# Optimization experiments

Measured on AMD Instinct MI355X. Metric: run time of the kernel, lower is better.

The kernel has to match this reference:

```python
import jax, jax.numpy as jnp
import numpy as np

B, T, V, E, H, N = 8, 128, 32000, 128, 256, 20
SHARPEN = 5.0
EPS = 1e-8  # torch cosine_similarity eps


def setup_inputs() -> dict:
    key = jax.random.key(0)
    ks = jax.random.split(key, 8)
    g = lambda k, shape, scale: (jax.random.normal(k, shape, dtype=jnp.float32) * scale)
    return {
        "x_ids": jax.random.randint(ks[0], (B, T), 0, V),
        "emb": g(ks[1], (V, E), 0.02),                 # nn.Embedding weight
        "W_i": g(ks[2], (H, E), E ** -0.5),            # rnn_i weight (no bias)
        "W_h": g(ks[3], (H, H), H ** -0.5),            # rnn_h weight
        "W_fc": g(ks[4], (V, 2 * H), (2 * H) ** -0.5), # fc -> vocab (softmaxed)
        "W_ops": g(ks[5], (3, 2 * H), (2 * H) ** -0.5),
        "W_choose": g(ks[6], (2, 2 * H), (2 * H) ** -0.5),
        "sharp": jnp.array([SHARPEN], dtype=jnp.float32),
    }


def _l2norm(x, eps=1e-12):
    # F.normalize(x, dim=-1)
    n = jnp.linalg.norm(x, axis=-1, keepdims=True)
    return x / jnp.maximum(n, eps)


def reference(x_ids, emb, W_i, W_h, W_fc, W_ops, W_choose, sharp):
    x = emb[x_ids]                                   # [B,T,E]
    # pre-normalize vocab rows for cosine-sim readout (clamped like torch)
    emb_cn = emb / jnp.maximum(jnp.linalg.norm(emb, axis=1, keepdims=True), EPS)
    sh = sharp[0]

    stack0 = jnp.full((B, N, E), 0.001, dtype=x.dtype)      # zero_offset + 0.001
    ptr0 = jnp.zeros((B, N), x.dtype).at[:, 0].set(1.0)     # pointer at slot 0
    h0 = jnp.zeros((B, H), x.dtype)

    def step(carry, xi):
        h, stack, ptr = carry
        ri = _l2norm(xi) @ W_i.T                     # rnn_i(normalize(x_t))
        h = jnp.tanh(ri + h @ W_h.T)
        hm = 1.0 - jax.nn.relu(h)
        hmod = jnp.concatenate([hm, hm], axis=1)     # [B,2H]
        # GumbelSoftmax(temp=1, hard=False) -> deterministic softmax (no noise)
        ops = jax.nn.softmax(hmod @ W_ops.T, axis=1)  # [B,3]
        push, pop, nop = ops[:, 0], ops[:, 1], ops[:, 2]
        # --- differentiable stack push/pop/nop ---
        pop_val = jnp.einsum('bn,bne->be', ptr, stack)      # soft read at pointer
        p_push = jnp.roll(ptr, 1, axis=1)
        p_pop = jnp.roll(ptr, -1, axis=1)
        new_ptr = push[:, None] * p_push + pop[:, None] * p_pop + nop[:, None] * ptr
        new_ptr = jnp.clip(new_ptr, EPS) ** sh              # sharpen
        new_ptr = new_ptr / jnp.sum(new_ptr, axis=1, keepdims=True)
        w = (push[:, None] * p_push)[:, :, None]            # write weight [B,N,1]
        new_stack = stack * (1.0 - w) + w * xi[:, None, :]
        # --- readout ---
        semantic = jax.nn.softmax(hmod @ W_fc.T, axis=1)    # [B,V]
        pv_n = pop_val / jnp.maximum(
            jnp.linalg.norm(pop_val, axis=1, keepdims=True), EPS)
        syntactic = pv_n @ emb_cn.T                          # cosine sim [B,V]
        choice = jax.nn.softmax(hmod @ W_choose.T, axis=1)   # [B,2]
        out = choice[:, 0:1] * semantic + choice[:, 1:2] * syntactic
        return (h, new_stack, new_ptr), out

    _, outs = jax.lax.scan(step, (h0, stack0, ptr0), jnp.swapaxes(x, 0, 1))
    return jnp.swapaxes(outs, 0, 1)  # [B,T,V]
```

## Files before the change

kernel.cpp:

```cpp
#include <hip/hip_runtime.h>
#include <hip/hip_bf16.h>
#include <stdint.h>

#define T_ 128
#define B_ 8
#define V_ 32000
#define E_ 128
#define H_ 256
#define N_ 20
#define M_ 1024
#define PIT 264
#define PIT2 136
#define NCH5 500

typedef __attribute__((ext_vector_type(8))) short short8;
typedef __attribute__((ext_vector_type(4))) float f32x4;
typedef unsigned short ushort;

static __device__ __forceinline__ ushort f2bf_u(float f) {
  __hip_bfloat16 h = __float2bfloat16(f);
  return *reinterpret_cast<ushort*>(&h);
}

__global__ void whb_k(const float* __restrict__ Wh, uint4* __restrict__ whb4) {
  int idx = blockIdx.x*256 + threadIdx.x;
  int k8 = idx >> 8, i = idx & 255;
  const float* s = Wh + i*H_ + k8*8;
  uint4 o;
  o.x = (uint32_t)f2bf_u(s[0]) | ((uint32_t)f2bf_u(s[1]) << 16);
  o.y = (uint32_t)f2bf_u(s[2]) | ((uint32_t)f2bf_u(s[3]) << 16);
  o.z = (uint32_t)f2bf_u(s[4]) | ((uint32_t)f2bf_u(s[5]) << 16);
  o.w = (uint32_t)f2bf_u(s[6]) | ((uint32_t)f2bf_u(s[7]) << 16);
  whb4[idx] = o;
}

__global__ void wit_k(const float* __restrict__ Wi, float* __restrict__ WiT) {
  int idx = blockIdx.x*256 + threadIdx.x;
  if (idx < H_*E_) {
    int i = idx >> 7, e = idx & (E_-1);
    WiT[e*H_ + i] = Wi[idx];
  }
}

__global__ void embn_k(const float* __restrict__ emb, ushort* __restrict__ embnb) {
  int v = blockIdx.x, l = threadIdx.x;
  float e0 = emb[v*E_ + l];
  float e1 = emb[v*E_ + 64 + l];
  float ss = e0*e0 + e1*e1;
  #pragma unroll
  for (int off = 32; off >= 1; off >>= 1) ss += __shfl_xor(ss, off);
  float inv = 1.f / fmaxf(sqrtf(ss), 1e-8f);
  embnb[v*E_ + l]      = f2bf_u(e0*inv);
  embnb[v*E_ + 64 + l] = f2bf_u(e1*inv);
}

__global__ void foldfc_k(const float* __restrict__ Wfc, ushort* __restrict__ Wfcb) {
  int idx = blockIdx.x*256 + threadIdx.x;
  int n = idx >> 8, k = idx & 255;
  Wfcb[idx] = f2bf_u(Wfc[n*2*H_ + k] + Wfc[n*2*H_ + H_ + k]);
}

__global__ __launch_bounds__(256) void ri_k(const int* __restrict__ x_ids,
    const float* __restrict__ emb, const float* __restrict__ WiT,
    float* __restrict__ RI)
{
  __shared__ float xn[E_];
  __shared__ float red[2];
  int r = blockIdx.x, tid = threadIdx.x;
  int id = x_ids[r];
  float v = 0.f;
  if (tid < E_) v = emb[id*E_ + tid];
  float ss = v*v;
  if (tid < E_) {
    #pragma unroll
    for (int off = 32; off >= 1; off >>= 1) ss += __shfl_xor(ss, off);
    if ((tid & 63) == 0) red[tid >> 6] = ss;
  }
  __syncthreads();
  float inv = 1.f / fmaxf(sqrtf(red[0] + red[1]), 1e-12f);
  if (tid < E_) xn[tid] = v*inv;
  __syncthreads();
  float s = 0.f;
  for (int e = 0; e < E_; ++e) s += xn[e]*WiT[e*H_ + tid];
  RI[r*H_ + tid] = s;
}

__global__ __launch_bounds__(1024) void chain_k(
    const uint4* __restrict__ whb4, const float* __restrict__ RI,
    float* __restrict__ HMf, ushort* __restrict__ HMb)
{
  __shared__ uint4 wlds[32*256];
  __shared__ __align__(16) float hbuf[2][H_];
  __shared__ float hred[3][H_];
  const int b = blockIdx.x, tid = threadIdx.x;
  const int q = tid >> 8, i = tid & 255;

  for (int m = tid; m < 32*256; m += 1024) wlds[m] = whb4[m];
  if (q == 0) hbuf[0][i] = 0.f;
  __syncthreads();
  float ri_c = (q == 0) ? RI[(size_t)b*T_*H_ + i] : 0.f;

  for (int t = 0; t < T_; ++t) {
    const int r = b*T_ + t;
    float ri_n = 0.f;
    if (q == 0 && t+1 < T_) ri_n = RI[(size_t)(r+1)*H_ + i];
    const float4* h4 = reinterpret_cast<const float4*>(hbuf[t & 1]);
    float p0 = 0.f, p1 = 0.f, p2 = 0.f, p3 = 0.f;
    #pragma unroll
    for (int j = 0; j < 8; ++j) {
      uint4 w = wlds[(q*8 + j)*256 + i];
      float4 ha = h4[q*16 + 2*j];
      float4 hb = h4[q*16 + 2*j + 1];
      p0 += __uint_as_float(w.x << 16)*ha.x + __uint_as_float(w.x & 0xffff0000u)*ha.y;
      p1 += __uint_as_float(w.y << 16)*ha.z + __uint_as_float(w.y & 0xffff0000u)*ha.w;
      p2 += __uint_as_float(w.z << 16)*hb.x + __uint_as_float(w.z & 0xffff0000u)*hb.y;
      p3 += __uint_as_float(w.w << 16)*hb.z + __uint_as_float(w.w & 0xffff0000u)*hb.w;
    }
    float p = (p0 + p1) + (p2 + p3);
    if (q) hred[q-1][i] = p;
    __syncthreads();
    if (q == 0) {
      float s = ri_c + p + hred[0][i] + hred[1][i] + hred[2][i];
      float hn = tanhf(s);
      hbuf[(t+1) & 1][i] = hn;
      float hm = 1.f - fmaxf(hn, 0.f);
      HMf[(size_t)r*H_ + i] = hm;
      HMb[(size_t)r*H_ + i] = f2bf_u(hm);
    }
    ri_c = ri_n;
    __syncthreads();
  }
}

__global__ __launch_bounds__(256) void stats5_k(const ushort* __restrict__ HMb,
    const ushort* __restrict__ Wfcb, const float* __restrict__ HMf,
    const float* __restrict__ W_ops, const float* __restrict__ W_ch,
    const float* __restrict__ sharp, const int* __restrict__ x_ids,
    const float* __restrict__ emb,
    float* __restrict__ SS, float* __restrict__ CH, float* __restrict__ PV,
    ushort* __restrict__ PVNb)
{
  __shared__ __align__(16) char smem[64*PIT*2];
  const int tid = threadIdx.x;
  const int wave = tid >> 6, lane = tid & 63;
  const int lr = lane & 15, g = lane >> 4;

  if (blockIdx.y == 0) {
    if (blockIdx.x >= B_) return;
    float*  ops_l = (float*)smem;
    float2* pw_l  = (float2*)(smem + 2048);
    int*    ids_l = (int*)(smem + 2048 + 20480);
    const int b = blockIdx.x;
    float wo[5][4];
    #pragma unroll
    for (int k = 0; k < 3; ++k)
      #pragma unroll
      for (int j = 0; j < 4; ++j)
        wo[k][j] = W_ops[k*2*H_ + 4*lane + j] + W_ops[k*2*H_ + H_ + 4*lane + j];
    #pragma unroll
    for (int k = 0; k < 2; ++k)
      #pragma unroll
      for (int j = 0; j < 4; ++j)
        wo[3+k][j] = W_ch[k*2*H_ + 4*lane + j] + W_ch[k*2*H_ + H_ + 4*lane + j];
    if (tid < T_) ids_l[tid] = x_ids[b*T_ + tid];
    for (int rl = wave*32; rl < wave*32 + 32; ++rl) {
      int R = b*T_ + rl;
      float4 hm4 = reinterpret_cast<const float4*>(HMf + (size_t)R*H_)[lane];
      float d0 = hm4.x*wo[0][0] + hm4.y*wo[0][1] + hm4.z*wo[0][2] + hm4.w*wo[0][3];
      float d1 = hm4.x*wo[1][0] + hm4.y*wo[1][1] + hm4.z*wo[1][2] + hm4.w*wo[1][3];
      float d2 = hm4.x*wo[2][0] + hm4.y*wo[2][1] + hm4.z*wo[2][2] + hm4.w*wo[2][3];
      float d3 = hm4.x*wo[3][0] + hm4.y*wo[3][1] + hm4.z*wo[3][2] + hm4.w*wo[3][3];
      float d4 = hm4.x*wo[4][0] + hm4.y*wo[4][1] + hm4.z*wo[4][2] + hm4.w*wo[4][3];
      #pragma unroll
      for (int off = 32; off >= 1; off >>= 1) {
        d0 += __shfl_xor(d0, off); d1 += __shfl_xor(d1, off); d2 += __shfl_xor(d2, off);
        d3 += __shfl_xor(d3, off); d4 += __shfl_xor(d4, off);
      }
      if (lane == 0) {
        float mx = fmaxf(d0, fmaxf(d1, d2));
        float e0 = expf(d0-mx), e1 = expf(d1-mx), e2 = expf(d2-mx);
        float oi = 1.f/(e0+e1+e2);
        ops_l[rl*4+0] = e0*oi; ops_l[rl*4+1] = e1*oi; ops_l[rl*4+2] = e2*oi;
        float cm = fmaxf(d3, d4);
        float f0 = expf(d3-cm), f1 = expf(d4-cm);
        float ci = 1.f/(f0+f1);
        CH[R*2] = f0*ci; CH[R*2+1] = f1*ci;
      }
    }
    __syncthreads();
    if (tid < 64) {
      const float sh = sharp[0];
      float ptr = (tid == 0) ? 1.f : 0.f;
      const int lp = (tid + N_ - 1) % N_, ln = (tid + 1) % N_;
      for (int t = 0; t < T_; ++t) {
        float push = ops_l[t*4+0], pop = ops_l[t*4+1], nop = ops_l[t*4+2];
        float pp = __shfl(ptr, lp);
        float po = __shfl(ptr, ln);
        float wgt = push*pp;
        float raw = wgt + pop*po + nop*ptr;
        float np = 0.f;
        if (tid < N_) np = exp2f(sh * log2f(fmaxf(raw, 1e-8f)));
        float ssum = np;
        #pragma unroll
        for (int off = 1; off < 32; off <<= 1) ssum += __shfl_xor(ssum, off);
        if (tid < N_) {
          pw_l[t*N_ + tid] = make_float2(ptr, wgt);
          ptr = np / ssum;
        }
      }
    }
    __syncthreads();
    if (tid < E_) {
      const int e = tid;
      float stck[N_];
      #pragma unroll
      for (int n = 0; n < N_; ++n) stck[n] = 0.001f;
      float xi_c = emb[(size_t)ids_l[0]*E_ + e];
      for (int t = 0; t < T_; ++t) {
        float xi_n = (t+1 < T_) ? emb[(size_t)ids_l[t+1]*E_ + e] : 0.f;
        float pv = 0.f;
        #pragma unroll
        for (int n = 0; n < N_; ++n) {
          float2 pw = pw_l[t*N_ + n];
          pv += pw.x * stck[n];
          stck[n] += pw.y * (xi_c - stck[n]);
        }
        PV[(size_t)(b*T_ + t)*E_ + e] = pv;
        xi_c = xi_n;
      }
    }
    __threadfence_block();
    __syncthreads();
    for (int rl = wave*32; rl < wave*32 + 32; ++rl) {
      int R = b*T_ + rl;
      float a = PV[(size_t)R*E_ + lane];
      float c = PV[(size_t)R*E_ + 64 + lane];
      float ss = a*a + c*c;
      #pragma unroll
      for (int off = 32; off >= 1; off >>= 1) ss += __shfl_xor(ss, off);
      float inv = 1.f / fmaxf(sqrtf(ss), 1e-8f);
      PVNb[(size_t)R*E_ + lane]      = f2bf_u(a*inv);
      PVNb[(size_t)R*E_ + 64 + lane] = f2bf_u(c*inv);
    }
    return;
  }

  ushort* Bs = (ushort*)smem;
  const int Cb = blockIdx.x*64;
  {
    const uint4* srcB = (const uint4*)(Wfcb + (size_t)Cb*H_);
    #pragma unroll
    for (int it = 0; it < 8; ++it) {
      int idx = it*256 + tid, row = idx >> 5, c = idx & 31;
      *(uint4*)&Bs[row*PIT + c*8] = srcB[row*32 + c];
    }
  }
  const int Rw = (blockIdx.y - 1)*128 + wave*32;
  short8 a[2][8];
  #pragma unroll
  for (int m = 0; m < 2; ++m)
    #pragma unroll
    for (int ks = 0; ks < 8; ++ks)
      a[m][ks] = *(const short8*)(HMb + (size_t)(Rw + m*16 + lr)*H_ + ks*32 + g*8);
  __syncthreads();
  f32x4 acc[2][4] = {};
  #pragma unroll
  for (int ks = 0; ks < 8; ++ks) {
    short8 b0 = *(const short8*)(&Bs[(0*16 + lr)*PIT + ks*32 + g*8]);
    short8 b1 = *(const short8*)(&Bs[(1*16 + lr)*PIT + ks*32 + g*8]);
    short8 b2 = *(const short8*)(&Bs[(2*16 + lr)*PIT + ks*32 + g*8]);
    short8 b3 = *(const short8*)(&Bs[(3*16 + lr)*PIT + ks*32 + g*8]);
    acc[0][0] = __builtin_amdgcn_mfma_f32_16x16x32_bf16(a[0][ks], b0, acc[0][0], 0, 0, 0);
    acc[0][1] = __builtin_amdgcn_mfma_f32_16x16x32_bf16(a[0][ks], b1, acc[0][1], 0, 0, 0);
    acc[0][2] = __builtin_amdgcn_mfma_f32_16x16x32_bf16(a[0][ks], b2, acc[0][2], 0, 0, 0);
    acc[0][3] = __builtin_amdgcn_mfma_f32_16x16x32_bf16(a[0][ks], b3, acc[0][3], 0, 0, 0);
    acc[1][0] = __builtin_amdgcn_mfma_f32_16x16x32_bf16(a[1][ks], b0, acc[1][0], 0, 0, 0);
    acc[1][1] = __builtin_amdgcn_mfma_f32_16x16x32_bf16(a[1][ks], b1, acc[1][1], 0, 0, 0);
    acc[1][2] = __builtin_amdgcn_mfma_f32_16x16x32_bf16(a[1][ks], b2, acc[1][2], 0, 0, 0);
    acc[1][3] = __builtin_amdgcn_mfma_f32_16x16x32_bf16(a[1][ks], b3, acc[1][3], 0, 0, 0);
  }
  #pragma unroll
  for (int mi = 0; mi < 2; ++mi)
    #pragma unroll
    for (int r = 0; r < 4; ++r) {
      float s = expf(acc[mi][0][r]) + expf(acc[mi][1][r])
              + expf(acc[mi][2][r]) + expf(acc[mi][3][r]);
      #pragma unroll
      for (int off = 1; off < 16; off <<= 1) s += __shfl_xor(s, off);
      if (lr == 0) SS[(size_t)blockIdx.x*M_ + (Rw + mi*16 + g*4 + r)] = s;
    }
}

__global__ void reduce5_k(const float* __restrict__ SS, float* __restrict__ MS) {
  int row = blockIdx.x, l = threadIdx.x;
  float s = 0.f;
  for (int c = l; c < NCH5; c += 64) s += SS[(size_t)c*M_ + row];
  #pragma unroll
  for (int off = 32; off >= 1; off >>= 1) s += __shfl_xor(s, off);
  if (l == 0) MS[row] = 1.f/s;
}

__global__ __launch_bounds__(256) void final5_k(const ushort* __restrict__ HMb,
    const ushort* __restrict__ Wfcb, const ushort* __restrict__ PVNb,
    const ushort* __restrict__ embnb, const float* __restrict__ MS,
    const float* __restrict__ CH, float* __restrict__ out)
{
  __shared__ __align__(16) ushort Bs[64*PIT];
  const int tid = threadIdx.x;
  const int Cb = blockIdx.x*64;
  const int wave = tid >> 6, lane = tid & 63;
  const int lr = lane & 15, g = lane >> 4;
  const int Rw = blockIdx.y*128 + wave*32;

  {
    const uint4* srcB = (const uint4*)(Wfcb + (size_t)Cb*H_);
    #pragma unroll
    for (int it = 0; it < 8; ++it) {
      int idx = it*256 + tid, row = idx >> 5, c = idx & 31;
      *(uint4*)&Bs[row*PIT + c*8] = srcB[row*32 + c];
    }
  }
  short8 a[2][8];
  #pragma unroll
  for (int m = 0; m < 2; ++m)
    #pragma unroll
    for (int ks = 0; ks < 8; ++ks)
      a[m][ks] = *(const short8*)(HMb + (size_t)(Rw + m*16 + lr)*H_ + ks*32 + g*8);
  __syncthreads();
  f32x4 accL[2][4] = {};
  #pragma unroll
  for (int ks = 0; ks < 8; ++ks) {
    short8 b0 = *(const short8*)(&Bs[(0*16 + lr)*PIT + ks*32 + g*8]);
    short8 b1 = *(const short8*)(&Bs[(1*16 + lr)*PIT + ks*32 + g*8]);
    short8 b2 = *(const short8*)(&Bs[(2*16 + lr)*PIT + ks*32 + g*8]);
    short8 b3 = *(const short8*)(&Bs[(3*16 + lr)*PIT + ks*32 + g*8]);
    accL[0][0] = __builtin_amdgcn_mfma_f32_16x16x32_bf16(a[0][ks], b0, accL[0][0], 0, 0, 0);
    accL[0][1] = __builtin_amdgcn_mfma_f32_16x16x32_bf16(a[0][ks], b1, accL[0][1], 0, 0, 0);
    accL[0][2] = __builtin_amdgcn_mfma_f32_16x16x32_bf16(a[0][ks], b2, accL[0][2], 0, 0, 0);
    accL[0][3] = __builtin_amdgcn_mfma_f32_16x16x32_bf16(a[0][ks], b3, accL[0][3], 0, 0, 0);
    accL[1][0] = __builtin_amdgcn_mfma_f32_16x16x32_bf16(a[1][ks], b0, accL[1][0], 0, 0, 0);
    accL[1][1] = __builtin_amdgcn_mfma_f32_16x16x32_bf16(a[1][ks], b1, accL[1][1], 0, 0, 0);
    accL[1][2] = __builtin_amdgcn_mfma_f32_16x16x32_bf16(a[1][ks], b2, accL[1][2], 0, 0, 0);
    accL[1][3] = __builtin_amdgcn_mfma_f32_16x16x32_bf16(a[1][ks], b3, accL[1][3], 0, 0, 0);
  }
  __syncthreads();

  {
    const uint4* srcB = (const uint4*)(embnb + (size_t)Cb*E_);
    #pragma unroll
    for (int it = 0; it < 4; ++it) {
      int idx = it*256 + tid, row = idx >> 4, c = idx & 15;
      *(uint4*)&Bs[row*PIT2 + c*8] = srcB[row*16 + c];
    }
  }
  short8 a2[2][4];
  #pragma unroll
  for (int m = 0; m < 2; ++m)
    #pragma unroll
    for (int ks = 0; ks < 4; ++ks)
      a2[m][ks] = *(const short8*)(PVNb + (size_t)(Rw + m*16 + lr)*E_ + ks*32 + g*8);
  __syncthreads();
  f32x4 accS[2][4] = {};
  #pragma unroll
  for (int ks = 0; ks < 4; ++ks) {
    short8 b0 = *(const short8*)(&Bs[(0*16 + lr)*PIT2 + ks*32 + g*8]);
    short8 b1 = *(const short8*)(&Bs[(1*16 + lr)*PIT2 + ks*32 + g*8]);
    short8 b2 = *(const short8*)(&Bs[(2*16 + lr)*PIT2 + ks*32 + g*8]);
    short8 b3 = *(const short8*)(&Bs[(3*16 + lr)*PIT2 + ks*32 + g*8]);
    accS[0][0] = __builtin_amdgcn_mfma_f32_16x16x32_bf16(a2[0][ks], b0, accS[0][0], 0, 0, 0);
    accS[0][1] = __builtin_amdgcn_mfma_f32_16x16x32_bf16(a2[0][ks], b1, accS[0][1], 0, 0, 0);
    accS[0][2] = __builtin_amdgcn_mfma_f32_16x16x32_bf16(a2[0][ks], b2, accS[0][2], 0, 0, 0);
    accS[0][3] = __builtin_amdgcn_mfma_f32_16x16x32_bf16(a2[0][ks], b3, accS[0][3], 0, 0, 0);
    accS[1][0] = __builtin_amdgcn_mfma_f32_16x16x32_bf16(a2[1][ks], b0, accS[1][0], 0, 0, 0);
    accS[1][1] = __builtin_amdgcn_mfma_f32_16x16x32_bf16(a2[1][ks], b1, accS[1][1], 0, 0, 0);
    accS[1][2] = __builtin_amdgcn_mfma_f32_16x16x32_bf16(a2[1][ks], b2, accS[1][2], 0, 0, 0);
    accS[1][3] = __builtin_amdgcn_mfma_f32_16x16x32_bf16(a2[1][ks], b3, accS[1][3], 0, 0, 0);
  }

  #pragma unroll
  for (int mi = 0; mi < 2; ++mi)
    #pragma unroll
    for (int r = 0; r < 4; ++r) {
      int row = Rw + mi*16 + g*4 + r;
      float Si = MS[row];
      float c0 = CH[row*2], c1 = CH[row*2+1];
      size_t base = (size_t)row*V_ + Cb + lr;
      #pragma unroll
      for (int nj = 0; nj < 4; ++nj)
        out[base + nj*16] = c0*expf(accL[mi][nj][r])*Si + c1*accS[mi][nj][r];
    }
}

extern "C" void kernel_launch(void* const* d_in, const int* in_sizes, int n_in,
                              void* d_out, int out_size, void* d_ws, size_t ws_size,
                              hipStream_t stream) {
  const int*   x_ids = (const int*)d_in[0];
  const float* emb   = (const float*)d_in[1];
  const float* W_i   = (const float*)d_in[2];
  const float* W_h   = (const float*)d_in[3];
  const float* W_fc  = (const float*)d_in[4];
  const float* W_ops = (const float*)d_in[5];
  const float* W_ch  = (const float*)d_in[6];
  const float* sharp = (const float*)d_in[7];
  float* out = (float*)d_out;

  float* ws    = (float*)d_ws;
  uint4*  whb4 = (uint4*)ws;
  float*  WiT  = ws + 65536;
  float*  RI   = WiT + 32768;
  float*  CH   = RI + 262144;
  float*  MS   = CH + 2048;
  float*  SS   = MS + 1024;
  float*  HMf  = SS + 512000;
  float*  PV   = HMf + 262144;
  float*  fend = PV + 131072;
  ushort* HMb   = (ushort*)fend;
  ushort* PVNb  = HMb + 262144;
  ushort* Wfcb  = PVNb + 131072;
  ushort* embnb = Wfcb + 8192000;

  whb_k  <<<32, 256, 0, stream>>>(W_h, whb4);
  wit_k  <<<(H_*E_ + 255)/256, 256, 0, stream>>>(W_i, WiT);
  embn_k <<<V_, 64, 0, stream>>>(emb, embnb);
  foldfc_k<<<V_*H_/256, 256, 0, stream>>>(W_fc, Wfcb);
  ri_k   <<<M_, 256, 0, stream>>>(x_ids, emb, WiT, RI);
  chain_k<<<B_, 1024, 0, stream>>>(whb4, RI, HMf, HMb);
  stats5_k<<<dim3(NCH5, 9), 256, 0, stream>>>(HMb, Wfcb, HMf, W_ops, W_ch, sharp,
                                              x_ids, emb, SS, CH, PV, PVNb);
  reduce5_k<<<M_, 64, 0, stream>>>(SS, MS);
  final5_k<<<dim3(NCH5, M_/128), 256, 0, stream>>>(HMb, Wfcb, PVNb, embnb, MS, CH, out);
}
```

Before: 422.8 us.

## Overlap weight prep with recurrent chain and enlarge GEMM row tiles

The separate embedding-normalize and W_fc fold/convert kernels are folded into extra blocks of the chain kernel. The chain kernel uses only 8 blocks, so this prep work can run on idle CUs while the sequential recurrence runs. Separately, the stats and final MFMA kernels now give each wave 64 rows instead of 32, so each LDS-staged Wfcb/embnb tile is reused across twice as many rows and the grid is halved in y. A operands are now loaded from global inside the k-loop rather than preloaded into registers, which adds register pressure from the larger accumulator arrays and may expose load latency.

```diff
diff --git a/kernel.cpp b/kernel.cpp
--- a/kernel.cpp
+++ b/kernel.cpp
@@ -40,24 +40,6 @@
     int i = idx >> 7, e = idx & (E_-1);
     WiT[e*H_ + i] = Wi[idx];
   }
-}
-
-__global__ void embn_k(const float* __restrict__ emb, ushort* __restrict__ embnb) {
-  int v = blockIdx.x, l = threadIdx.x;
-  float e0 = emb[v*E_ + l];
-  float e1 = emb[v*E_ + 64 + l];
-  float ss = e0*e0 + e1*e1;
-  #pragma unroll
-  for (int off = 32; off >= 1; off >>= 1) ss += __shfl_xor(ss, off);
-  float inv = 1.f / fmaxf(sqrtf(ss), 1e-8f);
-  embnb[v*E_ + l]      = f2bf_u(e0*inv);
-  embnb[v*E_ + 64 + l] = f2bf_u(e1*inv);
-}
-
-__global__ void foldfc_k(const float* __restrict__ Wfc, ushort* __restrict__ Wfcb) {
-  int idx = blockIdx.x*256 + threadIdx.x;
-  int n = idx >> 8, k = idx & 255;
-  Wfcb[idx] = f2bf_u(Wfc[n*2*H_ + k] + Wfc[n*2*H_ + H_ + k]);
 }
 
 __global__ __launch_bounds__(256) void ri_k(const int* __restrict__ x_ids,
@@ -87,12 +69,37 @@
 
 __global__ __launch_bounds__(1024) void chain_k(
     const uint4* __restrict__ whb4, const float* __restrict__ RI,
-    float* __restrict__ HMf, ushort* __restrict__ HMb)
+    float* __restrict__ HMf, ushort* __restrict__ HMb,
+    const float* __restrict__ Wfc, const float* __restrict__ emb,
+    ushort* __restrict__ Wfcb, ushort* __restrict__ embnb)
 {
   __shared__ uint4 wlds[32*256];
   __shared__ __align__(16) float hbuf[2][H_];
   __shared__ float hred[3][H_];
-  const int b = blockIdx.x, tid = threadIdx.x;
+  const int tid = threadIdx.x;
+
+  if (blockIdx.x >= B_) {
+    const int nb = gridDim.x - B_;
+    const int bx = blockIdx.x - B_;
+    for (long idx = (long)bx*1024 + tid; idx < (long)V_*H_; idx += (long)nb*1024) {
+      int n = idx >> 8, k = idx & 255;
+      Wfcb[idx] = f2bf_u(Wfc[(size_t)n*2*H_ + k] + Wfc[(size_t)n*2*H_ + H_ + k]);
+    }
+    const int wv = tid >> 6, l = tid & 63;
+    for (int v = bx*16 + wv; v < V_; v += nb*16) {
+      float e0 = emb[(size_t)v*E_ + l];
+      float e1 = emb[(size_t)v*E_ + 64 + l];
+      float ss = e0*e0 + e1*e1;
+      #pragma unroll
+      for (int off = 32; off >= 1; off >>= 1) ss += __shfl_xor(ss, off);
+      float inv = 1.f / fmaxf(sqrtf(ss), 1e-8f);
+      embnb[(size_t)v*E_ + l]      = f2bf_u(e0*inv);
+      embnb[(size_t)v*E_ + 64 + l] = f2bf_u(e1*inv);
+    }
+    return;
+  }
+
+  const int b = blockIdx.x;
   const int q = tid >> 8, i = tid & 255;
 
   for (int m = tid; m < 32*256; m += 1024) wlds[m] = whb4[m];
@@ -132,7 +139,7 @@
   }
 }
 
-__global__ __launch_bounds__(256) void stats5_k(const ushort* __restrict__ HMb,
+__global__ __launch_bounds__(256) void stats6_k(const ushort* __restrict__ HMb,
     const ushort* __restrict__ Wfcb, const float* __restrict__ HMf,
     const float* __restrict__ W_ops, const float* __restrict__ W_ch,
     const float* __restrict__ sharp, const int* __restrict__ x_ids,
@@ -255,32 +262,29 @@
       *(uint4*)&Bs[row*PIT + c*8] = srcB[row*32 + c];
     }
   }
-  const int Rw = (blockIdx.y - 1)*128 + wave*32;
-  short8 a[2][8];
-  #pragma unroll
-  for (int m = 0; m < 2; ++m)
-    #pragma unroll
-    for (int ks = 0; ks < 8; ++ks)
-      a[m][ks] = *(const short8*)(HMb + (size_t)(Rw + m*16 + lr)*H_ + ks*32 + g*8);
-  __syncthreads();
-  f32x4 acc[2][4] = {};
+  const int Rw = (blockIdx.y - 1)*256 + wave*64;
+  __syncthreads();
+  f32x4 acc[4][4] = {};
   #pragma unroll
   for (int ks = 0; ks < 8; ++ks) {
+    short8 a0 = *(const short8*)(HMb + (size_t)(Rw + 0*16 + lr)*H_ + ks*32 + g*8);
+    short8 a1 = *(const short8*)(HMb + (size_t)(Rw + 1*16 + lr)*H_ + ks*32 + g*8);
+    short8 a2 = *(const short8*)(HMb + (size_t)(Rw + 2*16 + lr)*H_ + ks*32 + g*8);
+    short8 a3 = *(const short8*)(HMb + (size_t)(Rw + 3*16 + lr)*H_ + ks*32 + g*8);
     short8 b0 = *(const short8*)(&Bs[(0*16 + lr)*PIT + ks*32 + g*8]);
     short8 b1 = *(const short8*)(&Bs[(1*16 + lr)*PIT + ks*32 + g*8]);
     short8 b2 = *(const short8*)(&Bs[(2*16 + lr)*PIT + ks*32 + g*8]);
     short8 b3 = *(const short8*)(&Bs[(3*16 + lr)*PIT + ks*32 + g*8]);
-    acc[0][0] = __builtin_amdgcn_mfma_f32_16x16x32_bf16(a[0][ks], b0, acc[0][0], 0, 0, 0);
-    acc[0][1] = __builtin_amdgcn_mfma_f32_16x16x32_bf16(a[0][ks], b1, acc[0][1], 0, 0, 0);
-    acc[0][2] = __builtin_amdgcn_mfma_f32_16x16x32_bf16(a[0][ks], b2, acc[0][2], 0, 0, 0);
-    acc[0][3] = __builtin_amdgcn_mfma_f32_16x16x32_bf16(a[0][ks], b3, acc[0][3], 0, 0, 0);
-    acc[1][0] = __builtin_amdgcn_mfma_f32_16x16x32_bf16(a[1][ks], b0, acc[1][0], 0, 0, 0);
-    acc[1][1] = __builtin_amdgcn_mfma_f32_16x16x32_bf16(a[1][ks], b1, acc[1][1], 0, 0, 0);
-    acc[1][2] = __builtin_amdgcn_mfma_f32_16x16x32_bf16(a[1][ks], b2, acc[1][2], 0, 0, 0);
-    acc[1][3] = __builtin_amdgcn_mfma_f32_16x16x32_bf16(a[1][ks], b3, acc[1][3], 0, 0, 0);
-  }
-  #pragma unroll
-  for (int mi = 0; mi < 2; ++mi)
+    #define MF(mi, av) \
+      acc[mi][0] = __builtin_amdgcn_mfma_f32_16x16x32_bf16(av, b0, acc[mi][0], 0, 0, 0); \
+      acc[mi][1] = __builtin_amdgcn_mfma_f32_16x16x32_bf16(av, b1, acc[mi][1], 0, 0, 0); \
+      acc[mi][2] = __builtin_amdgcn_mfma_f32_16x16x32_bf16(av, b2, acc[mi][2], 0, 0, 0); \
+      acc[mi][3] = __builtin_amdgcn_mfma_f32_16x16x32_bf16(av, b3, acc[mi][3], 0, 0, 0);
+    MF(0, a0) MF(1, a1) MF(2, a2) MF(3, a3)
+    #undef MF
+  }
+  #pragma unroll
+  for (int mi = 0; mi < 4; ++mi)
     #pragma unroll
     for (int r = 0; r < 4; ++r) {
       float s = expf(acc[mi][0][r]) + expf(acc[mi][1][r])
@@ -300,7 +304,7 @@
   if (l == 0) MS[row] = 1.f/s;
 }
 
-__global__ __launch_bounds__(256) void final5_k(const ushort* __restrict__ HMb,
+__global__ __launch_bounds__(256) void final6_k(const ushort* __restrict__ HMb,
     const ushort* __restrict__ Wfcb, const ushort* __restrict__ PVNb,
     const ushort* __restrict__ embnb, const float* __restrict__ MS,
     const float* __restrict__ CH, float* __restrict__ out)
@@ -310,7 +314,7 @@
   const int Cb = blockIdx.x*64;
   const int wave = tid >> 6, lane = tid & 63;
   const int lr = lane & 15, g = lane >> 4;
-  const int Rw = blockIdx.y*128 + wave*32;
+  const int Rw = blockIdx.y*256 + wave*64;
 
   {
     const uint4* srcB = (const uint4*)(Wfcb + (size_t)Cb*H_);
@@ -320,28 +324,25 @@
       *(uint4*)&Bs[row*PIT + c*8] = srcB[row*32 + c];
     }
   }
-  short8 a[2][8];
-  #pragma unroll
-  for (int m = 0; m < 2; ++m)
-    #pragma unroll
-    for (int ks = 0; ks < 8; ++ks)
-      a[m][ks] = *(const short8*)(HMb + (size_t)(Rw + m*16 + lr)*H_ + ks*32 + g*8);
-  __syncthreads();
-  f32x4 accL[2][4] = {};
+  __syncthreads();
+  f32x4 accL[4][4] = {};
   #pragma unroll
   for (int ks = 0; ks < 8; ++ks) {
+    short8 a0 = *(const short8*)(HMb + (size_t)(Rw + 0*16 + lr)*H_ + ks*32 + g*8);
+    short8 a1 = *(const short8*)(HMb + (size_t)(Rw + 1*16 + lr)*H_ + ks*32 + g*8);
+    short8 a2 = *(const short8*)(HMb + (size_t)(Rw + 2*16 + lr)*H_ + ks*32 + g*8);
+    short8 a3 = *(const short8*)(HMb + (size_t)(Rw + 3*16 + lr)*H_ + ks*32 + g*8);
     short8 b0 = *(const short8*)(&Bs[(0*16 + lr)*PIT + ks*32 + g*8]);
     short8 b1 = *(const short8*)(&Bs[(1*16 + lr)*PIT + ks*32 + g*8]);
     short8 b2 = *(const short8*)(&Bs[(2*16 + lr)*PIT + ks*32 + g*8]);
     short8 b3 = *(const short8*)(&Bs[(3*16 + lr)*PIT + ks*32 + g*8]);
-    accL[0][0] = __builtin_amdgcn_mfma_f32_16x16x32_bf16(a[0][ks], b0, accL[0][0], 0, 0, 0);
-    accL[0][1] = __builtin_amdgcn_mfma_f32_16x16x32_bf16(a[0][ks], b1, accL[0][1], 0, 0, 0);
-    accL[0][2] = __builtin_amdgcn_mfma_f32_16x16x32_bf16(a[0][ks], b2, accL[0][2], 0, 0, 0);
-    accL[0][3] = __builtin_amdgcn_mfma_f32_16x16x32_bf16(a[0][ks], b3, accL[0][3], 0, 0, 0);
-    accL[1][0] = __builtin_amdgcn_mfma_f32_16x16x32_bf16(a[1][ks], b0, accL[1][0], 0, 0, 0);
-    accL[1][1] = __builtin_amdgcn_mfma_f32_16x16x32_bf16(a[1][ks], b1, accL[1][1], 0, 0, 0);
-    accL[1][2] = __builtin_amdgcn_mfma_f32_16x16x32_bf16(a[1][ks], b2, accL[1][2], 0, 0, 0);
-    accL[1][3] = __builtin_amdgcn_mfma_f32_16x16x32_bf16(a[1][ks], b3, accL[1][3], 0, 0, 0);
+    #define MFL(mi, av) \
+      accL[mi][0] = __builtin_amdgcn_mfma_f32_16x16x32_bf16(av, b0, accL[mi][0], 0, 0, 0); \
+      accL[mi][1] = __builtin_amdgcn_mfma_f32_16x16x32_bf16(av, b1, accL[mi][1], 0, 0, 0); \
+      accL[mi][2] = __builtin_amdgcn_mfma_f32_16x16x32_bf16(av, b2, accL[mi][2], 0, 0, 0); \
+      accL[mi][3] = __builtin_amdgcn_mfma_f32_16x16x32_bf16(av, b3, accL[mi][3], 0, 0, 0);
+    MFL(0, a0) MFL(1, a1) MFL(2, a2) MFL(3, a3)
+    #undef MFL
   }
   __syncthreads();
 
@@ -353,32 +354,29 @@
       *(uint4*)&Bs[row*PIT2 + c*8] = srcB[row*16 + c];
     }
   }
-  short8 a2[2][4];
-  #pragma unroll
-  for (int m = 0; m < 2; ++m)
-    #pragma unroll
-    for (int ks = 0; ks < 4; ++ks)
-      a2[m][ks] = *(const short8*)(PVNb + (size_t)(Rw + m*16 + lr)*E_ + ks*32 + g*8);
-  __syncthreads();
-  f32x4 accS[2][4] = {};
+  __syncthreads();
+  f32x4 accS[4][4] = {};
   #pragma unroll
   for (int ks = 0; ks < 4; ++ks) {
+    short8 a0 = *(const short8*)(PVNb + (size_t)(Rw + 0*16 + lr)*E_ + ks*32 + g*8);
+    short8 a1 = *(const short8*)(PVNb + (size_t)(Rw + 1*16 + lr)*E_ + ks*32 + g*8);
+    short8 a2 = *(const short8*)(PVNb + (size_t)(Rw + 2*16 + lr)*E_ + ks*32 + g*8);
+    short8 a3 = *(const short8*)(PVNb + (size_t)(Rw + 3*16 + lr)*E_ + ks*32 + g*8);
     short8 b0 = *(const short8*)(&Bs[(0*16 + lr)*PIT2 + ks*32 + g*8]);
     short8 b1 = *(const short8*)(&Bs[(1*16 + lr)*PIT2 + ks*32 + g*8]);
     short8 b2 = *(const short8*)(&Bs[(2*16 + lr)*PIT2 + ks*32 + g*8]);
     short8 b3 = *(const short8*)(&Bs[(3*16 + lr)*PIT2 + ks*32 + g*8]);
-    accS[0][0] = __builtin_amdgcn_mfma_f32_16x16x32_bf16(a2[0][ks], b0, accS[0][0], 0, 0, 0);
-    accS[0][1] = __builtin_amdgcn_mfma_f32_16x16x32_bf16(a2[0][ks], b1, accS[0][1], 0, 0, 0);
-    accS[0][2] = __builtin_amdgcn_mfma_f32_16x16x32_bf16(a2[0][ks], b2, accS[0][2], 0, 0, 0);
-    accS[0][3] = __builtin_amdgcn_mfma_f32_16x16x32_bf16(a2[0][ks], b3, accS[0][3], 0, 0, 0);
-    accS[1][0] = __builtin_amdgcn_mfma_f32_16x16x32_bf16(a2[1][ks], b0, accS[1][0], 0, 0, 0);
-    accS[1][1] = __builtin_amdgcn_mfma_f32_16x16x32_bf16(a2[1][ks], b1, accS[1][1], 0, 0, 0);
-    accS[1][2] = __builtin_amdgcn_mfma_f32_16x16x32_bf16(a2[1][ks], b2, accS[1][2], 0, 0, 0);
-    accS[1][3] = __builtin_amdgcn_mfma_f32_16x16x32_bf16(a2[1][ks], b3, accS[1][3], 0, 0, 0);
-  }
-
-  #pragma unroll
-  for (int mi = 0; mi < 2; ++mi)
+    #define MFS(mi, av) \
+      accS[mi][0] = __builtin_amdgcn_mfma_f32_16x16x32_bf16(av, b0, accS[mi][0], 0, 0, 0); \
+      accS[mi][1] = __builtin_amdgcn_mfma_f32_16x16x32_bf16(av, b1, accS[mi][1], 0, 0, 0); \
+      accS[mi][2] = __builtin_amdgcn_mfma_f32_16x16x32_bf16(av, b2, accS[mi][2], 0, 0, 0); \
+      accS[mi][3] = __builtin_amdgcn_mfma_f32_16x16x32_bf16(av, b3, accS[mi][3], 0, 0, 0);
+    MFS(0, a0) MFS(1, a1) MFS(2, a2) MFS(3, a3)
+    #undef MFS
+  }
+
+  #pragma unroll
+  for (int mi = 0; mi < 4; ++mi)
     #pragma unroll
     for (int r = 0; r < 4; ++r) {
       int row = Rw + mi*16 + g*4 + r;
@@ -421,12 +419,10 @@
 
   whb_k  <<<32, 256, 0, stream>>>(W_h, whb4);
   wit_k  <<<(H_*E_ + 255)/256, 256, 0, stream>>>(W_i, WiT);
-  embn_k <<<V_, 64, 0, stream>>>(emb, embnb);
-  foldfc_k<<<V_*H_/256, 256, 0, stream>>>(W_fc, Wfcb);
   ri_k   <<<M_, 256, 0, stream>>>(x_ids, emb, WiT, RI);
-  chain_k<<<B_, 1024, 0, stream>>>(whb4, RI, HMf, HMb);
-  stats5_k<<<dim3(NCH5, 9), 256, 0, stream>>>(HMb, Wfcb, HMf, W_ops, W_ch, sharp,
+  chain_k<<<248, 1024, 0, stream>>>(whb4, RI, HMf, HMb, W_fc, emb, Wfcb, embnb);
+  stats6_k<<<dim3(NCH5, 5), 256, 0, stream>>>(HMb, Wfcb, HMf, W_ops, W_ch, sharp,
                                               x_ids, emb, SS, CH, PV, PVNb);
   reduce5_k<<<M_, 64, 0, stream>>>(SS, MS);
-  final5_k<<<dim3(NCH5, M_/128), 256, 0, stream>>>(HMb, Wfcb, PVNb, embnb, MS, CH, out);
-}
+  final6_k<<<dim3(NCH5, M_/256), 256, 0, stream>>>(HMb, Wfcb, PVNb, embnb, MS, CH, out);
+}
```

Measured after the change: 383.7 us. 1.1x faster.
